# Performance work log

Measured on AMD Instinct MI355X. Metric: run time of the kernel, lower is better.

The kernel has to match this reference:

```python
import jax, jax.numpy as jnp
import numpy as np

B, N, D, H_DIM = 8, 100, 768, 768
TH = 24            # 384 / patch16
IMG = 384


def setup_inputs() -> dict:
    key = jax.random.key(0)
    k0, k1, k2, k3 = jax.random.split(key, 4)
    patch_tokens = jax.random.normal(k0, (B, TH * TH + 1, D), jnp.float32)
    raw = jax.random.uniform(k1, (B, N, 4), jnp.float32)
    x1 = jnp.minimum(raw[..., 0], raw[..., 2])
    x2 = jnp.maximum(raw[..., 0], raw[..., 2])
    y1 = jnp.minimum(raw[..., 1], raw[..., 3])
    y2 = jnp.maximum(raw[..., 1], raw[..., 3])
    boxes = jnp.stack([x1, y1, x2, y2], axis=-1)
    W1 = jax.random.normal(k2, (2 * D, H_DIM), jnp.float32) * 0.02
    b1 = jnp.zeros((H_DIM,), jnp.float32)
    W2 = jax.random.normal(k3, (H_DIM, 1), jnp.float32) * 0.02
    b2 = jnp.zeros((1,), jnp.float32)
    return {"patch_tokens": patch_tokens, "boxes": boxes, "W1": W1, "b1": b1,
            "W2": W2, "b2": b2, "img_h": IMG, "img_w": IMG}


def reference(patch_tokens, boxes, W1, b1, W2, b2, img_h, img_w):
    Bt, T, Dm = patch_tokens.shape
    th = int(T ** 0.5)                       # token_hw (24 for T=577)
    seq = patch_tokens[:, 1:, :] if T == th * th + 1 else patch_tokens
    feat_map = seq.reshape(Bt, th, th, Dm)   # [B, th, th, D]

    # --- box -> patch-grid coordinates (replicates int() truncation chain) ---
    def to_patch(v, size):
        pix = jnp.floor(v * size)            # int(x * W), x >= 0
        return jnp.floor(pix / size * th).astype(jnp.int32)

    px1 = jnp.clip(to_patch(boxes[..., 0], img_w), 0, th - 1)  # [B, N]
    py1 = jnp.clip(to_patch(boxes[..., 1], img_h), 0, th - 1)
    px2 = jnp.clip(to_patch(boxes[..., 2], img_w), 1, th)
    py2 = jnp.clip(to_patch(boxes[..., 3], img_h), 1, th)
    # empty-region fallback: single cell at (py1, px1)
    px2 = jnp.where(px2 > px1, px2, px1 + 1)
    py2 = jnp.where(py2 > py1, py2, py1 + 1)

    # --- vectorized ROI mean pooling via rectangle masks ---
    ar = jnp.arange(th)
    mx = (ar[None, None, :] >= px1[..., None]) & (ar[None, None, :] < px2[..., None])  # [B,N,th]
    my = (ar[None, None, :] >= py1[..., None]) & (ar[None, None, :] < py2[..., None])  # [B,N,th]
    mask = (my[..., :, None] & mx[..., None, :]).astype(feat_map.dtype)               # [B,N,th,th]
    count = mask.sum(axis=(-1, -2))                                                   # [B,N]
    pooled = jnp.einsum('bnhw,bhwd->bnd', mask, feat_map) / count[..., None]          # [B,N,D]

    # --- pairwise concat-MLP: cat([fi, fj]) @ W1 == fi @ W1[:D] + fj @ W1[D:] ---
    ha = pooled @ W1[:Dm]                     # [B,N,H]
    hb = pooled @ W1[Dm:]                     # [B,N,H]
    hid = jax.nn.relu(ha[:, :, None, :] + hb[:, None, :, :] + b1)  # [B,N,N,H]
    logits = (hid @ W2)[..., 0] + b2[0]       # [B,N,N]
    return jax.nn.sigmoid(logits)
```

## Files before the change

kernel.cpp:

```cpp
#include <hip/hip_runtime.h>
#include <hip/hip_bf16.h>
#include <math.h>

#define PB   8
#define PN   100
#define PD   768
#define PT   577
#define PTH  24
#define BN_TOT (PB * PN)
#define MPAD   832

typedef __attribute__((ext_vector_type(8))) short bf16x8;
typedef __attribute__((ext_vector_type(4))) float f32x4;

#define SATX_BLOCKS 144
#define CVT_BLOCKS  1152

__global__ __launch_bounds__(256) void prep_kernel(
    const float* __restrict__ patch,
    const float* __restrict__ W1,
    float* __restrict__ SAT,
    __hip_bfloat16* __restrict__ W1T)
{
    __shared__ float tile[32][33];
    const int t = threadIdx.x;

    if (blockIdx.x < SATX_BLOCKS) {
        const int gid = blockIdx.x * 256 + t;
        const int d4 = gid % 192;
        const int y  = (gid / 192) % PTH;
        const int b  = gid / (192 * PTH);

        const float4* src = (const float4*)(patch + ((size_t)(b * PT + 1 + y * PTH)) * PD) + d4;
        float4* dst = (float4*)(SAT + ((size_t)((b * 25) + (y + 1)) * 25) * PD) + d4;

        dst[0] = make_float4(0.f, 0.f, 0.f, 0.f);
        float4 acc = make_float4(0.f, 0.f, 0.f, 0.f);
#pragma unroll
        for (int X = 1; X <= PTH; ++X) {
            float4 v = src[(size_t)(X - 1) * 192];
            acc.x += v.x; acc.y += v.y; acc.z += v.z; acc.w += v.w;
            dst[(size_t)X * 192] = acc;
        }
    } else {
        const int bid = blockIdx.x - SATX_BLOCKS;
        const int half = bid / 576;
        const int rem  = bid % 576;
        const int k0 = (rem / 24) * 32;
        const int n0 = (rem % 24) * 32;
        const int c  = t & 31;
        const int r4 = t >> 5;

#pragma unroll
        for (int l = 0; l < 4; ++l) {
            int r = r4 + 8 * l;
            tile[r][c] = W1[(size_t)(half * PD + k0 + r) * PD + n0 + c];
        }
        __syncthreads();
#pragma unroll
        for (int l = 0; l < 4; ++l) {
            int r = r4 + 8 * l;
            W1T[(size_t)(half * PD + n0 + r) * PD + k0 + c] =
                __float2bfloat16(tile[c][r]);
        }
    }
}

__global__ __launch_bounds__(256) void sat_y_kernel(float* __restrict__ SAT)
{
    const int gid = blockIdx.x * 256 + threadIdx.x;
    const int d4 = gid % 192;
    const int X  = (gid / 192) % 25;
    const int b  = gid / (192 * 25);

    float4* col = (float4*)(SAT + ((size_t)(b * 25) * 25 + X) * PD) + d4;
    col[0] = make_float4(0.f, 0.f, 0.f, 0.f);
    float4 acc = make_float4(0.f, 0.f, 0.f, 0.f);
#pragma unroll
    for (int Y = 1; Y <= PTH; ++Y) {
        float4* p = col + (size_t)Y * 25 * 192;
        float4 v = *p;
        acc.x += v.x; acc.y += v.y; acc.z += v.z; acc.w += v.w;
        *p = acc;
    }
}

__global__ __launch_bounds__(192) void pool_sat_kernel(
    const float* __restrict__ SAT,
    const float* __restrict__ boxes,
    const int*   __restrict__ img_h,
    const int*   __restrict__ img_w,
    __hip_bfloat16* __restrict__ pooledh)
{
    const int m = blockIdx.x;
    const int t = threadIdx.x;
    short4* o = (short4*)(pooledh + (size_t)m * PD);

    if (m >= BN_TOT) {
        short4 z; z.x = 0; z.y = 0; z.z = 0; z.w = 0;
        o[t] = z;
        return;
    }

    const int b = m / PN;
    const float x1 = boxes[m * 4 + 0];
    const float y1 = boxes[m * 4 + 1];
    const float x2 = boxes[m * 4 + 2];
    const float y2 = boxes[m * 4 + 3];
    const float W  = (float)img_w[0];
    const float H  = (float)img_h[0];

    auto to_patch = [](float v, float size) -> int {
        float pix = floorf(v * size);
        float tt  = pix / size * (float)PTH;
        return (int)floorf(tt);
    };
    int px1 = min(max(to_patch(x1, W), 0), PTH - 1);
    int py1 = min(max(to_patch(y1, H), 0), PTH - 1);
    int px2 = min(max(to_patch(x2, W), 1), PTH);
    int py2 = min(max(to_patch(y2, H), 1), PTH);
    if (px2 <= px1) px2 = px1 + 1;
    if (py2 <= py1) py2 = py1 + 1;
    const float inv = 1.0f / (float)((px2 - px1) * (py2 - py1));

    const float* Sb = SAT + (size_t)b * 25 * 25 * PD;
    const float4 s22 = ((const float4*)(Sb + ((size_t)py2 * 25 + px2) * PD))[t];
    const float4 s12 = ((const float4*)(Sb + ((size_t)py1 * 25 + px2) * PD))[t];
    const float4 s21 = ((const float4*)(Sb + ((size_t)py2 * 25 + px1) * PD))[t];
    const float4 s11 = ((const float4*)(Sb + ((size_t)py1 * 25 + px1) * PD))[t];

    auto cvt = [](float f) -> short {
        __hip_bfloat16 h = __float2bfloat16(f);
        return *(short*)&h;
    };
    short4 r;
    r.x = cvt(((s22.x - s12.x) - (s21.x - s11.x)) * inv);
    r.y = cvt(((s22.y - s12.y) - (s21.y - s11.y)) * inv);
    r.z = cvt(((s22.z - s12.z) - (s21.z - s11.z)) * inv);
    r.w = cvt(((s22.w - s12.w) - (s21.w - s11.w)) * inv);
    o[t] = r;
}

__global__ __launch_bounds__(128) void gemm_mfma_kernel(
    const __hip_bfloat16* __restrict__ A,
    const __hip_bfloat16* __restrict__ Bt,
    const float* __restrict__ b1,
    float* __restrict__ C)
{
    const int bn = blockIdx.x;
    const int bm = blockIdx.y;
    const int wave = threadIdx.x >> 6;
    const int lane = threadIdx.x & 63;
    const int lm = lane & 15;
    const int g  = lane >> 4;

    const int m0 = bm * 32;
    const int n0 = bn * 64 + wave * 32;

    const __hip_bfloat16* pa0 = A  + (size_t)(m0 + lm) * PD + g * 8;
    const __hip_bfloat16* pa1 = pa0 + (size_t)16 * PD;
    const __hip_bfloat16* pb0 = Bt + (size_t)(n0 + lm) * PD + g * 8;
    const __hip_bfloat16* pb1 = pb0 + (size_t)16 * PD;

    f32x4 acc00 = {}, acc01 = {}, acc10 = {}, acc11 = {};

#pragma unroll 4
    for (int k0 = 0; k0 < PD; k0 += 32) {
        bf16x8 a0 = *(const bf16x8*)(pa0 + k0);
        bf16x8 a1 = *(const bf16x8*)(pa1 + k0);
        bf16x8 b0 = *(const bf16x8*)(pb0 + k0);
        bf16x8 b1v = *(const bf16x8*)(pb1 + k0);
        acc00 = __builtin_amdgcn_mfma_f32_16x16x32_bf16(a0, b0,  acc00, 0, 0, 0);
        acc01 = __builtin_amdgcn_mfma_f32_16x16x32_bf16(a0, b1v, acc01, 0, 0, 0);
        acc10 = __builtin_amdgcn_mfma_f32_16x16x32_bf16(a1, b0,  acc10, 0, 0, 0);
        acc11 = __builtin_amdgcn_mfma_f32_16x16x32_bf16(a1, b1v, acc11, 0, 0, 0);
    }

    const int rbase = g * 4;
#pragma unroll
    for (int r = 0; r < 4; ++r) {
        int row0 = m0 + rbase + r;
        int row1 = row0 + 16;
        int col0 = n0 + lm;
        int col1 = col0 + 16;
        float bb0 = (col0 < PD) ? b1[col0] : 0.0f;
        float bb1 = (col1 < PD) ? b1[col1] : 0.0f;
        C[(size_t)row0 * 1536 + col0] = acc00[r] + bb0;
        C[(size_t)row0 * 1536 + col1] = acc01[r] + bb1;
        C[(size_t)row1 * 1536 + col0] = acc10[r] + bb0;
        C[(size_t)row1 * 1536 + col1] = acc11[r] + bb1;
    }
}

__device__ __forceinline__ float rdot(const float4 A, const float4 C,
                                      const float4 W, float s) {
    s = fmaf(fmaxf(A.x + C.x, 0.f), W.x, s);
    s = fmaf(fmaxf(A.y + C.y, 0.f), W.y, s);
    s = fmaf(fmaxf(A.z + C.z, 0.f), W.z, s);
    s = fmaf(fmaxf(A.w + C.w, 0.f), W.w, s);
    return s;
}

__global__ __launch_bounds__(256) void pair_kernel(
    const float* __restrict__ hab,
    const float* __restrict__ W2,
    const float* __restrict__ b2,
    float* __restrict__ out)
{
    const int jt = blockIdx.x;
    const int i0 = blockIdx.y * 8;
    const int b  = blockIdx.z;
    const int nrows = min(8, PN - i0);
    const int t = threadIdx.x;
    const int wave = t >> 6;
    const int lane = t & 63;

    const float4* w2v = (const float4*)W2;
    const float4 w0 = w2v[lane], w1 = w2v[lane + 64], w2r = w2v[lane + 128];
    const float bb2 = b2[0];

    float4 a[8][3];
#pragma unroll
    for (int i = 0; i < 8; ++i) {
        int row = b * PN + (i < nrows ? i0 + i : i0);
        const float4* ha = (const float4*)(hab + (size_t)row * 1536);
        a[i][0] = ha[lane]; a[i][1] = ha[lane + 64]; a[i][2] = ha[lane + 128];
    }

    const float4* hbbase = (const float4*)(hab + (size_t)(b * PN) * 1536) + 192;
    const int jend = jt * 50 + 50;
    int j = jt * 50 + wave;

    float4 h0, h1, h2;
    {
        const float4* hb = hbbase + (size_t)j * 384;
        h0 = hb[lane]; h1 = hb[lane + 64]; h2 = hb[lane + 128];
    }

    for (; j < jend; j += 4) {
        const float4 c0 = h0, c1 = h1, c2 = h2;
        const int jn = j + 4;
        if (jn < jend) {
            const float4* hb = hbbase + (size_t)jn * 384;
            h0 = hb[lane]; h1 = hb[lane + 64]; h2 = hb[lane + 128];
        }
        float acc[8];
#pragma unroll
        for (int i = 0; i < 8; ++i)
            acc[i] = rdot(a[i][2], c2, w2r, rdot(a[i][1], c1, w1, rdot(a[i][0], c0, w0, 0.f)));
#pragma unroll
        for (int i = 0; i < 8; ++i)
#pragma unroll
            for (int m = 32; m; m >>= 1)
                acc[i] += __shfl_xor(acc[i], m, 64);
        if (lane == 0) {
#pragma unroll
            for (int i = 0; i < 8; ++i)
                if (i < nrows)
                    out[(size_t)(b * PN + i0 + i) * PN + j] =
                        1.0f / (1.0f + expf(-(acc[i] + bb2)));
        }
    }
}

extern "C" void kernel_launch(void* const* d_in, const int* in_sizes, int n_in,
                              void* d_out, int out_size, void* d_ws, size_t ws_size,
                              hipStream_t stream) {
    const float* patch = (const float*)d_in[0];
    const float* boxes = (const float*)d_in[1];
    const float* W1    = (const float*)d_in[2];
    const float* b1    = (const float*)d_in[3];
    const float* W2    = (const float*)d_in[4];
    const float* b2    = (const float*)d_in[5];
    const int*   img_h = (const int*)d_in[6];
    const int*   img_w = (const int*)d_in[7];
    float* out = (float*)d_out;

    char* wsb = (char*)d_ws;
    float*          SAT     = (float*)(wsb);
    __hip_bfloat16* pooledh = (__hip_bfloat16*)(wsb + 15360000);
    __hip_bfloat16* W1T     = (__hip_bfloat16*)(wsb + 15360000 + 1277952);
    float*          hab     = (float*)(wsb + 15360000 + 1277952 + 2359296);

    prep_kernel<<<SATX_BLOCKS + CVT_BLOCKS, 256, 0, stream>>>(patch, W1, SAT, W1T);
    sat_y_kernel<<<150, 256, 0, stream>>>(SAT);
    pool_sat_kernel<<<MPAD, 192, 0, stream>>>(SAT, boxes, img_h, img_w, pooledh);
    gemm_mfma_kernel<<<dim3(24, 26), 128, 0, stream>>>(pooledh, W1T, b1, hab);
    pair_kernel<<<dim3(2, 13, 8), 256, 0, stream>>>(hab, W2, b2, out);
}
```

Baseline: 137.5 us.

## Fuse all stages into one persistent kernel with grid-wide atomic barriers

Merges the prep, pooling, GEMM and pairwise kernels into a single persistent launch of 416 blocks, separated by software grid barriers built on atomic counters in the workspace. The counters are reset with a memset before each launch. The 2D summed-area table is replaced by row-wise prefix sums only, so each box is pooled by looping over its rows instead of using a four-corner lookup. The GEMM and pair stages are re-tiled so each fits the fixed block count. The change targets launch overhead and the separate vertical-scan pass, at the cost of barrier spin and the risk of deadlock if not all blocks are co-resident.

```diff
diff --git a/kernel.cpp b/kernel.cpp
--- a/kernel.cpp
+++ b/kernel.cpp
@@ -7,189 +7,38 @@
 #define PD   768
 #define PT   577
 #define PTH  24
-#define BN_TOT (PB * PN)
+#define BN_TOT 800
 #define MPAD   832
+
+#define NBLK 416
+#define NTHR 256
+#define TOTTHR (NBLK * NTHR)
 
 typedef __attribute__((ext_vector_type(8))) short bf16x8;
 typedef __attribute__((ext_vector_type(4))) float f32x4;
 
-#define SATX_BLOCKS 144
-#define CVT_BLOCKS  1152
-
-__global__ __launch_bounds__(256) void prep_kernel(
-    const float* __restrict__ patch,
-    const float* __restrict__ W1,
-    float* __restrict__ SAT,
-    __hip_bfloat16* __restrict__ W1T)
-{
-    __shared__ float tile[32][33];
-    const int t = threadIdx.x;
-
-    if (blockIdx.x < SATX_BLOCKS) {
-        const int gid = blockIdx.x * 256 + t;
-        const int d4 = gid % 192;
-        const int y  = (gid / 192) % PTH;
-        const int b  = gid / (192 * PTH);
-
-        const float4* src = (const float4*)(patch + ((size_t)(b * PT + 1 + y * PTH)) * PD) + d4;
-        float4* dst = (float4*)(SAT + ((size_t)((b * 25) + (y + 1)) * 25) * PD) + d4;
-
-        dst[0] = make_float4(0.f, 0.f, 0.f, 0.f);
-        float4 acc = make_float4(0.f, 0.f, 0.f, 0.f);
-#pragma unroll
-        for (int X = 1; X <= PTH; ++X) {
-            float4 v = src[(size_t)(X - 1) * 192];
-            acc.x += v.x; acc.y += v.y; acc.z += v.z; acc.w += v.w;
-            dst[(size_t)X * 192] = acc;
-        }
-    } else {
-        const int bid = blockIdx.x - SATX_BLOCKS;
-        const int half = bid / 576;
-        const int rem  = bid % 576;
-        const int k0 = (rem / 24) * 32;
-        const int n0 = (rem % 24) * 32;
-        const int c  = t & 31;
-        const int r4 = t >> 5;
-
-#pragma unroll
-        for (int l = 0; l < 4; ++l) {
-            int r = r4 + 8 * l;
-            tile[r][c] = W1[(size_t)(half * PD + k0 + r) * PD + n0 + c];
-        }
-        __syncthreads();
-#pragma unroll
-        for (int l = 0; l < 4; ++l) {
-            int r = r4 + 8 * l;
-            W1T[(size_t)(half * PD + n0 + r) * PD + k0 + c] =
-                __float2bfloat16(tile[c][r]);
-        }
-    }
-}
-
-__global__ __launch_bounds__(256) void sat_y_kernel(float* __restrict__ SAT)
-{
-    const int gid = blockIdx.x * 256 + threadIdx.x;
-    const int d4 = gid % 192;
-    const int X  = (gid / 192) % 25;
-    const int b  = gid / (192 * 25);
-
-    float4* col = (float4*)(SAT + ((size_t)(b * 25) * 25 + X) * PD) + d4;
-    col[0] = make_float4(0.f, 0.f, 0.f, 0.f);
-    float4 acc = make_float4(0.f, 0.f, 0.f, 0.f);
-#pragma unroll
-    for (int Y = 1; Y <= PTH; ++Y) {
-        float4* p = col + (size_t)Y * 25 * 192;
-        float4 v = *p;
-        acc.x += v.x; acc.y += v.y; acc.z += v.z; acc.w += v.w;
-        *p = acc;
-    }
-}
-
-__global__ __launch_bounds__(192) void pool_sat_kernel(
-    const float* __restrict__ SAT,
-    const float* __restrict__ boxes,
-    const int*   __restrict__ img_h,
-    const int*   __restrict__ img_w,
-    __hip_bfloat16* __restrict__ pooledh)
-{
-    const int m = blockIdx.x;
-    const int t = threadIdx.x;
-    short4* o = (short4*)(pooledh + (size_t)m * PD);
-
-    if (m >= BN_TOT) {
-        short4 z; z.x = 0; z.y = 0; z.z = 0; z.w = 0;
-        o[t] = z;
-        return;
-    }
-
-    const int b = m / PN;
-    const float x1 = boxes[m * 4 + 0];
-    const float y1 = boxes[m * 4 + 1];
-    const float x2 = boxes[m * 4 + 2];
-    const float y2 = boxes[m * 4 + 3];
-    const float W  = (float)img_w[0];
-    const float H  = (float)img_h[0];
-
-    auto to_patch = [](float v, float size) -> int {
-        float pix = floorf(v * size);
-        float tt  = pix / size * (float)PTH;
-        return (int)floorf(tt);
-    };
-    int px1 = min(max(to_patch(x1, W), 0), PTH - 1);
-    int py1 = min(max(to_patch(y1, H), 0), PTH - 1);
-    int px2 = min(max(to_patch(x2, W), 1), PTH);
-    int py2 = min(max(to_patch(y2, H), 1), PTH);
-    if (px2 <= px1) px2 = px1 + 1;
-    if (py2 <= py1) py2 = py1 + 1;
-    const float inv = 1.0f / (float)((px2 - px1) * (py2 - py1));
-
-    const float* Sb = SAT + (size_t)b * 25 * 25 * PD;
-    const float4 s22 = ((const float4*)(Sb + ((size_t)py2 * 25 + px2) * PD))[t];
-    const float4 s12 = ((const float4*)(Sb + ((size_t)py1 * 25 + px2) * PD))[t];
-    const float4 s21 = ((const float4*)(Sb + ((size_t)py2 * 25 + px1) * PD))[t];
-    const float4 s11 = ((const float4*)(Sb + ((size_t)py1 * 25 + px1) * PD))[t];
-
-    auto cvt = [](float f) -> short {
-        __hip_bfloat16 h = __float2bfloat16(f);
-        return *(short*)&h;
-    };
-    short4 r;
-    r.x = cvt(((s22.x - s12.x) - (s21.x - s11.x)) * inv);
-    r.y = cvt(((s22.y - s12.y) - (s21.y - s11.y)) * inv);
-    r.z = cvt(((s22.z - s12.z) - (s21.z - s11.z)) * inv);
-    r.w = cvt(((s22.w - s12.w) - (s21.w - s11.w)) * inv);
-    o[t] = r;
-}
-
-__global__ __launch_bounds__(128) void gemm_mfma_kernel(
-    const __hip_bfloat16* __restrict__ A,
-    const __hip_bfloat16* __restrict__ Bt,
-    const float* __restrict__ b1,
-    float* __restrict__ C)
-{
-    const int bn = blockIdx.x;
-    const int bm = blockIdx.y;
-    const int wave = threadIdx.x >> 6;
-    const int lane = threadIdx.x & 63;
-    const int lm = lane & 15;
-    const int g  = lane >> 4;
-
-    const int m0 = bm * 32;
-    const int n0 = bn * 64 + wave * 32;
-
-    const __hip_bfloat16* pa0 = A  + (size_t)(m0 + lm) * PD + g * 8;
-    const __hip_bfloat16* pa1 = pa0 + (size_t)16 * PD;
-    const __hip_bfloat16* pb0 = Bt + (size_t)(n0 + lm) * PD + g * 8;
-    const __hip_bfloat16* pb1 = pb0 + (size_t)16 * PD;
-
-    f32x4 acc00 = {}, acc01 = {}, acc10 = {}, acc11 = {};
-
-#pragma unroll 4
-    for (int k0 = 0; k0 < PD; k0 += 32) {
-        bf16x8 a0 = *(const bf16x8*)(pa0 + k0);
-        bf16x8 a1 = *(const bf16x8*)(pa1 + k0);
-        bf16x8 b0 = *(const bf16x8*)(pb0 + k0);
-        bf16x8 b1v = *(const bf16x8*)(pb1 + k0);
-        acc00 = __builtin_amdgcn_mfma_f32_16x16x32_bf16(a0, b0,  acc00, 0, 0, 0);
-        acc01 = __builtin_amdgcn_mfma_f32_16x16x32_bf16(a0, b1v, acc01, 0, 0, 0);
-        acc10 = __builtin_amdgcn_mfma_f32_16x16x32_bf16(a1, b0,  acc10, 0, 0, 0);
-        acc11 = __builtin_amdgcn_mfma_f32_16x16x32_bf16(a1, b1v, acc11, 0, 0, 0);
-    }
-
-    const int rbase = g * 4;
-#pragma unroll
-    for (int r = 0; r < 4; ++r) {
-        int row0 = m0 + rbase + r;
-        int row1 = row0 + 16;
-        int col0 = n0 + lm;
-        int col1 = col0 + 16;
-        float bb0 = (col0 < PD) ? b1[col0] : 0.0f;
-        float bb1 = (col1 < PD) ? b1[col1] : 0.0f;
-        C[(size_t)row0 * 1536 + col0] = acc00[r] + bb0;
-        C[(size_t)row0 * 1536 + col1] = acc01[r] + bb1;
-        C[(size_t)row1 * 1536 + col0] = acc10[r] + bb0;
-        C[(size_t)row1 * 1536 + col1] = acc11[r] + bb1;
-    }
+#define OFF_POOLED 14745600
+#define OFF_W1T    16023552
+#define OFF_HAB    18382848
+#define OFF_BAR    23494656
+
+__device__ __forceinline__ void gbar(unsigned* cnt, unsigned* flag) {
+    __syncthreads();
+    if (threadIdx.x == 0) {
+        __threadfence();
+        unsigned prev = __hip_atomic_fetch_add(cnt, 1u, __ATOMIC_ACQ_REL,
+                                               __HIP_MEMORY_SCOPE_AGENT);
+        if (prev == NBLK - 1) {
+            __hip_atomic_store(flag, 1u, __ATOMIC_RELEASE,
+                               __HIP_MEMORY_SCOPE_AGENT);
+        } else {
+            while (__hip_atomic_load(flag, __ATOMIC_ACQUIRE,
+                                     __HIP_MEMORY_SCOPE_AGENT) == 0u)
+                __builtin_amdgcn_s_sleep(2);
+        }
+        __threadfence();
+    }
+    __syncthreads();
 }
 
 __device__ __forceinline__ float rdot(const float4 A, const float4 C,
@@ -201,64 +50,218 @@
     return s;
 }
 
-__global__ __launch_bounds__(256) void pair_kernel(
-    const float* __restrict__ hab,
+__global__ __launch_bounds__(NTHR, 2) void fused_kernel(
+    const float* __restrict__ patch,
+    const float* __restrict__ boxes,
+    const float* __restrict__ W1,
+    const float* __restrict__ b1,
     const float* __restrict__ W2,
     const float* __restrict__ b2,
-    float* __restrict__ out)
+    const int*   __restrict__ img_h,
+    const int*   __restrict__ img_w,
+    float* __restrict__ out,
+    char* __restrict__ wsb)
 {
-    const int jt = blockIdx.x;
-    const int i0 = blockIdx.y * 8;
-    const int b  = blockIdx.z;
-    const int nrows = min(8, PN - i0);
-    const int t = threadIdx.x;
-    const int wave = t >> 6;
-    const int lane = t & 63;
-
-    const float4* w2v = (const float4*)W2;
-    const float4 w0 = w2v[lane], w1 = w2v[lane + 64], w2r = w2v[lane + 128];
-    const float bb2 = b2[0];
-
-    float4 a[8][3];
-#pragma unroll
-    for (int i = 0; i < 8; ++i) {
-        int row = b * PN + (i < nrows ? i0 + i : i0);
-        const float4* ha = (const float4*)(hab + (size_t)row * 1536);
-        a[i][0] = ha[lane]; a[i][1] = ha[lane + 64]; a[i][2] = ha[lane + 128];
-    }
-
-    const float4* hbbase = (const float4*)(hab + (size_t)(b * PN) * 1536) + 192;
-    const int jend = jt * 50 + 50;
-    int j = jt * 50 + wave;
-
-    float4 h0, h1, h2;
+    __shared__ float tile[32][33];
+
+    float*          Sx      = (float*)(wsb);
+    __hip_bfloat16* pooledh = (__hip_bfloat16*)(wsb + OFF_POOLED);
+    __hip_bfloat16* W1T     = (__hip_bfloat16*)(wsb + OFF_W1T);
+    float*          hab     = (float*)(wsb + OFF_HAB);
+    unsigned*       bar     = (unsigned*)(wsb + OFF_BAR);
+
+    const int bid = blockIdx.x;
+    const int t   = threadIdx.x;
+
+    if (bid < 144) {
+        const int gid = bid * 256 + t;
+        const int d4 = gid % 192;
+        const int y  = (gid / 192) % PTH;
+        const int b  = gid / (192 * PTH);
+
+        const float4* src = (const float4*)(patch +
+                            ((size_t)(b * PT + 1 + y * PTH)) * PD);
+        float4* dst = (float4*)(Sx + ((size_t)(b * PTH + y) * 25) * PD) + d4;
+
+        dst[0] = make_float4(0.f, 0.f, 0.f, 0.f);
+        float4 acc = make_float4(0.f, 0.f, 0.f, 0.f);
+#pragma unroll
+        for (int X = 1; X <= PTH; ++X) {
+            float4 v = src[(size_t)(X - 1) * 192 + d4];
+            acc.x += v.x; acc.y += v.y; acc.z += v.z; acc.w += v.w;
+            dst[(size_t)X * 192] = acc;
+        }
+    } else {
+        for (int tl = bid - 144; tl < 1152; tl += NBLK - 144) {
+            const int hf  = tl / 576;
+            const int rem = tl % 576;
+            const int k0 = (rem / 24) * 32;
+            const int n0 = (rem % 24) * 32;
+            const int c  = t & 31;
+            const int r4 = t >> 5;
+#pragma unroll
+            for (int l = 0; l < 4; ++l) {
+                int r = r4 + 8 * l;
+                tile[r][c] = W1[(size_t)(hf * PD + k0 + r) * PD + n0 + c];
+            }
+            __syncthreads();
+#pragma unroll
+            for (int l = 0; l < 4; ++l) {
+                int r = r4 + 8 * l;
+                W1T[(size_t)(hf * PD + n0 + r) * PD + k0 + c] =
+                    __float2bfloat16(tile[c][r]);
+            }
+            __syncthreads();
+        }
+    }
+    gbar(bar + 0, bar + 32);
+
     {
-        const float4* hb = hbbase + (size_t)j * 384;
-        h0 = hb[lane]; h1 = hb[lane + 64]; h2 = hb[lane + 128];
-    }
-
-    for (; j < jend; j += 4) {
-        const float4 c0 = h0, c1 = h1, c2 = h2;
-        const int jn = j + 4;
-        if (jn < jend) {
-            const float4* hb = hbbase + (size_t)jn * 384;
+        const float Wf = (float)img_w[0];
+        const float Hf = (float)img_h[0];
+        for (int u = bid * 256 + t; u < MPAD * 192; u += TOTTHR) {
+            const int m  = u / 192;
+            const int d4 = u % 192;
+            short4* o = (short4*)(pooledh + (size_t)m * PD) + d4;
+            if (m >= BN_TOT) {
+                short4 z; z.x = 0; z.y = 0; z.z = 0; z.w = 0;
+                *o = z;
+                continue;
+            }
+            const int b = m / PN;
+            auto to_patch = [](float v, float size) -> int {
+                float pix = floorf(v * size);
+                float tt  = pix / size * (float)PTH;
+                return (int)floorf(tt);
+            };
+            int px1 = min(max(to_patch(boxes[m * 4 + 0], Wf), 0), PTH - 1);
+            int py1 = min(max(to_patch(boxes[m * 4 + 1], Hf), 0), PTH - 1);
+            int px2 = min(max(to_patch(boxes[m * 4 + 2], Wf), 1), PTH);
+            int py2 = min(max(to_patch(boxes[m * 4 + 3], Hf), 1), PTH);
+            if (px2 <= px1) px2 = px1 + 1;
+            if (py2 <= py1) py2 = py1 + 1;
+            const float inv = 1.0f / (float)((px2 - px1) * (py2 - py1));
+
+            const float* Sb = Sx + (size_t)b * PTH * 25 * PD;
+            float4 s = make_float4(0.f, 0.f, 0.f, 0.f);
+            for (int y = py1; y < py2; ++y) {
+                const float4* r2 = (const float4*)(Sb + ((size_t)y * 25 + px2) * PD) + d4;
+                const float4* r1 = (const float4*)(Sb + ((size_t)y * 25 + px1) * PD) + d4;
+                float4 a2 = *r2, a1 = *r1;
+                s.x += a2.x - a1.x; s.y += a2.y - a1.y;
+                s.z += a2.z - a1.z; s.w += a2.w - a1.w;
+            }
+            auto cvt = [](float f) -> short {
+                __hip_bfloat16 h = __float2bfloat16(f);
+                return *(short*)&h;
+            };
+            short4 r;
+            r.x = cvt(s.x * inv); r.y = cvt(s.y * inv);
+            r.z = cvt(s.z * inv); r.w = cvt(s.w * inv);
+            *o = r;
+        }
+    }
+    gbar(bar + 64, bar + 96);
+
+    if (bid < 312) {
+        const int bm = bid / 24;
+        const int bn = bid % 24;
+        const int wave = t >> 6;
+        const int lane = t & 63;
+        const int lm = lane & 15;
+        const int g  = lane >> 4;
+        const int m0 = bm * 64 + (wave >> 1) * 32;
+        const int n0 = bn * 64 + (wave & 1) * 32;
+
+        const __hip_bfloat16* pa0 = pooledh + (size_t)(m0 + lm) * PD + g * 8;
+        const __hip_bfloat16* pa1 = pa0 + (size_t)16 * PD;
+        const __hip_bfloat16* pb0 = W1T + (size_t)(n0 + lm) * PD + g * 8;
+        const __hip_bfloat16* pb1 = pb0 + (size_t)16 * PD;
+
+        f32x4 acc00 = {}, acc01 = {}, acc10 = {}, acc11 = {};
+#pragma unroll 4
+        for (int k0 = 0; k0 < PD; k0 += 32) {
+            bf16x8 a0 = *(const bf16x8*)(pa0 + k0);
+            bf16x8 a1 = *(const bf16x8*)(pa1 + k0);
+            bf16x8 b0 = *(const bf16x8*)(pb0 + k0);
+            bf16x8 b1v = *(const bf16x8*)(pb1 + k0);
+            acc00 = __builtin_amdgcn_mfma_f32_16x16x32_bf16(a0, b0,  acc00, 0, 0, 0);
+            acc01 = __builtin_amdgcn_mfma_f32_16x16x32_bf16(a0, b1v, acc01, 0, 0, 0);
+            acc10 = __builtin_amdgcn_mfma_f32_16x16x32_bf16(a1, b0,  acc10, 0, 0, 0);
+            acc11 = __builtin_amdgcn_mfma_f32_16x16x32_bf16(a1, b1v, acc11, 0, 0, 0);
+        }
+        const int rbase = g * 4;
+#pragma unroll
+        for (int r = 0; r < 4; ++r) {
+            int row0 = m0 + rbase + r;
+            int row1 = row0 + 16;
+            int col0 = n0 + lm;
+            int col1 = col0 + 16;
+            float bb0 = (col0 < PD) ? b1[col0] : 0.0f;
+            float bb1 = (col1 < PD) ? b1[col1] : 0.0f;
+            hab[(size_t)row0 * 1536 + col0] = acc00[r] + bb0;
+            hab[(size_t)row0 * 1536 + col1] = acc01[r] + bb1;
+            hab[(size_t)row1 * 1536 + col0] = acc10[r] + bb0;
+            hab[(size_t)row1 * 1536 + col1] = acc11[r] + bb1;
+        }
+    }
+    gbar(bar + 128, bar + 160);
+
+    {
+        const int jt = bid & 3;
+        const int it = (bid >> 2) % 13;
+        const int b  = bid / 52;
+        const int i0 = it * 8;
+        const int nrows = min(8, PN - i0);
+        const int wave = t >> 6;
+        const int lane = t & 63;
+
+        const float4* w2v = (const float4*)W2;
+        const float4 w0 = w2v[lane], w1 = w2v[lane + 64], w2r = w2v[lane + 128];
+        const float bb2 = b2[0];
+
+        float4 a[8][3];
+#pragma unroll
+        for (int i = 0; i < 8; ++i) {
+            int row = b * PN + (i < nrows ? i0 + i : i0);
+            const float4* ha = (const float4*)(hab + (size_t)row * 1536);
+            a[i][0] = ha[lane]; a[i][1] = ha[lane + 64]; a[i][2] = ha[lane + 128];
+        }
+
+        const float4* hbbase = (const float4*)(hab + (size_t)(b * PN) * 1536) + 192;
+        const int jend = jt * 25 + 25;
+        int j = jt * 25 + wave;
+
+        float4 h0, h1, h2;
+        {
+            const float4* hb = hbbase + (size_t)j * 384;
             h0 = hb[lane]; h1 = hb[lane + 64]; h2 = hb[lane + 128];
         }
-        float acc[8];
-#pragma unroll
-        for (int i = 0; i < 8; ++i)
-            acc[i] = rdot(a[i][2], c2, w2r, rdot(a[i][1], c1, w1, rdot(a[i][0], c0, w0, 0.f)));
-#pragma unroll
-        for (int i = 0; i < 8; ++i)
-#pragma unroll
-            for (int m = 32; m; m >>= 1)
-                acc[i] += __shfl_xor(acc[i], m, 64);
-        if (lane == 0) {
+        for (; j < jend; j += 4) {
+            const float4 c0 = h0, c1 = h1, c2 = h2;
+            const int jn = j + 4;
+            if (jn < jend) {
+                const float4* hb = hbbase + (size_t)jn * 384;
+                h0 = hb[lane]; h1 = hb[lane + 64]; h2 = hb[lane + 128];
+            }
+            float acc[8];
 #pragma unroll
             for (int i = 0; i < 8; ++i)
-                if (i < nrows)
-                    out[(size_t)(b * PN + i0 + i) * PN + j] =
-                        1.0f / (1.0f + expf(-(acc[i] + bb2)));
+                acc[i] = rdot(a[i][2], c2, w2r,
+                         rdot(a[i][1], c1, w1,
+                         rdot(a[i][0], c0, w0, 0.f)));
+#pragma unroll
+            for (int i = 0; i < 8; ++i)
+#pragma unroll
+                for (int m = 32; m; m >>= 1)
+                    acc[i] += __shfl_xor(acc[i], m, 64);
+            if (lane == 0) {
+#pragma unroll
+                for (int i = 0; i < 8; ++i)
+                    if (i < nrows)
+                        out[(size_t)(b * PN + i0 + i) * PN + j] =
+                            1.0f / (1.0f + expf(-(acc[i] + bb2)));
+            }
         }
     }
 }
@@ -275,16 +278,9 @@
     const int*   img_h = (const int*)d_in[6];
     const int*   img_w = (const int*)d_in[7];
     float* out = (float*)d_out;
-
     char* wsb = (char*)d_ws;
-    float*          SAT     = (float*)(wsb);
-    __hip_bfloat16* pooledh = (__hip_bfloat16*)(wsb + 15360000);
-    __hip_bfloat16* W1T     = (__hip_bfloat16*)(wsb + 15360000 + 1277952);
-    float*          hab     = (float*)(wsb + 15360000 + 1277952 + 2359296);
-
-    prep_kernel<<<SATX_BLOCKS + CVT_BLOCKS, 256, 0, stream>>>(patch, W1, SAT, W1T);
-    sat_y_kernel<<<150, 256, 0, stream>>>(SAT);
-    pool_sat_kernel<<<MPAD, 192, 0, stream>>>(SAT, boxes, img_h, img_w, pooledh);
-    gemm_mfma_kernel<<<dim3(24, 26), 128, 0, stream>>>(pooledh, W1T, b1, hab);
-    pair_kernel<<<dim3(2, 13, 8), 256, 0, stream>>>(hab, W2, b2, out);
-}
+
+    hipMemsetAsync(wsb + OFF_BAR, 0, 1024, stream);
+    fused_kernel<<<NBLK, NTHR, 0, stream>>>(patch, boxes, W1, b1, W2, b2,
+                                            img_h, img_w, out, wsb);
+}
```

Measured after the change: 358.0 us. +160.4%, slower.

## Replace SAT pooling with direct box summation fused into W1 conversion kernel

Applied to the files above, without the earlier changes.

Drops the two-pass summed-area-table build (SAT x and y kernels plus the separate pool kernel) and sums each box's patch tokens directly inside one kernel. That kernel also carries the W1 transpose/bf16 conversion as a grid-stride loop, cutting three launches down to one and removing the 15 MB SAT workspace traffic. The pair kernel's j-range is split into 4 chunks instead of 2, doubling its grid for more parallelism. The trade-off is that direct summation costs work proportional to box area: large boxes can read up to 576 tokens each, which may load-imbalance blocks.

```diff
diff --git a/kernel.cpp b/kernel.cpp
--- a/kernel.cpp
+++ b/kernel.cpp
@@ -7,138 +7,88 @@
 #define PD   768
 #define PT   577
 #define PTH  24
-#define BN_TOT (PB * PN)
+#define BN_TOT 800
 #define MPAD   832
 
 typedef __attribute__((ext_vector_type(8))) short bf16x8;
 typedef __attribute__((ext_vector_type(4))) float f32x4;
 
-#define SATX_BLOCKS 144
-#define CVT_BLOCKS  1152
-
-__global__ __launch_bounds__(256) void prep_kernel(
+__global__ __launch_bounds__(256) void pool_prep_kernel(
     const float* __restrict__ patch,
+    const float* __restrict__ boxes,
     const float* __restrict__ W1,
-    float* __restrict__ SAT,
+    const int*   __restrict__ img_h,
+    const int*   __restrict__ img_w,
+    __hip_bfloat16* __restrict__ pooledh,
     __hip_bfloat16* __restrict__ W1T)
 {
     __shared__ float tile[32][33];
+    const int m = blockIdx.x;
     const int t = threadIdx.x;
 
-    if (blockIdx.x < SATX_BLOCKS) {
-        const int gid = blockIdx.x * 256 + t;
-        const int d4 = gid % 192;
-        const int y  = (gid / 192) % PTH;
-        const int b  = gid / (192 * PTH);
-
-        const float4* src = (const float4*)(patch + ((size_t)(b * PT + 1 + y * PTH)) * PD) + d4;
-        float4* dst = (float4*)(SAT + ((size_t)((b * 25) + (y + 1)) * 25) * PD) + d4;
-
-        dst[0] = make_float4(0.f, 0.f, 0.f, 0.f);
-        float4 acc = make_float4(0.f, 0.f, 0.f, 0.f);
-#pragma unroll
-        for (int X = 1; X <= PTH; ++X) {
-            float4 v = src[(size_t)(X - 1) * 192];
-            acc.x += v.x; acc.y += v.y; acc.z += v.z; acc.w += v.w;
-            dst[(size_t)X * 192] = acc;
-        }
-    } else {
-        const int bid = blockIdx.x - SATX_BLOCKS;
-        const int half = bid / 576;
-        const int rem  = bid % 576;
+    if (t < 192) {
+        short4* o = (short4*)(pooledh + (size_t)m * PD) + t;
+        if (m >= BN_TOT) {
+            short4 z; z.x = 0; z.y = 0; z.z = 0; z.w = 0;
+            *o = z;
+        } else {
+            const int b = m / PN;
+            const float Wf = (float)img_w[0];
+            const float Hf = (float)img_h[0];
+            auto to_patch = [](float v, float size) -> int {
+                float pix = floorf(v * size);
+                float tt  = pix / size * (float)PTH;
+                return (int)floorf(tt);
+            };
+            int px1 = min(max(to_patch(boxes[m * 4 + 0], Wf), 0), PTH - 1);
+            int py1 = min(max(to_patch(boxes[m * 4 + 1], Hf), 0), PTH - 1);
+            int px2 = min(max(to_patch(boxes[m * 4 + 2], Wf), 1), PTH);
+            int py2 = min(max(to_patch(boxes[m * 4 + 3], Hf), 1), PTH);
+            if (px2 <= px1) px2 = px1 + 1;
+            if (py2 <= py1) py2 = py1 + 1;
+            const float inv = 1.0f / (float)((px2 - px1) * (py2 - py1));
+
+            const float* pb_ = patch + (size_t)(b * PT + 1) * PD;
+            float4 s = make_float4(0.f, 0.f, 0.f, 0.f);
+            for (int y = py1; y < py2; ++y) {
+                const float* rowp = pb_ + (size_t)(y * PTH) * PD;
+                for (int x = px1; x < px2; ++x) {
+                    float4 v = ((const float4*)(rowp + (size_t)x * PD))[t];
+                    s.x += v.x; s.y += v.y; s.z += v.z; s.w += v.w;
+                }
+            }
+            auto cvt = [](float f) -> short {
+                __hip_bfloat16 h = __float2bfloat16(f);
+                return *(short*)&h;
+            };
+            short4 r;
+            r.x = cvt(s.x * inv); r.y = cvt(s.y * inv);
+            r.z = cvt(s.z * inv); r.w = cvt(s.w * inv);
+            *o = r;
+        }
+    }
+
+    for (int tl = m; tl < 1152; tl += MPAD) {
+        const int hf  = tl / 576;
+        const int rem = tl % 576;
         const int k0 = (rem / 24) * 32;
         const int n0 = (rem % 24) * 32;
         const int c  = t & 31;
         const int r4 = t >> 5;
-
+        __syncthreads();
 #pragma unroll
         for (int l = 0; l < 4; ++l) {
             int r = r4 + 8 * l;
-            tile[r][c] = W1[(size_t)(half * PD + k0 + r) * PD + n0 + c];
+            tile[r][c] = W1[(size_t)(hf * PD + k0 + r) * PD + n0 + c];
         }
         __syncthreads();
 #pragma unroll
         for (int l = 0; l < 4; ++l) {
             int r = r4 + 8 * l;
-            W1T[(size_t)(half * PD + n0 + r) * PD + k0 + c] =
+            W1T[(size_t)(hf * PD + n0 + r) * PD + k0 + c] =
                 __float2bfloat16(tile[c][r]);
         }
     }
-}
-
-__global__ __launch_bounds__(256) void sat_y_kernel(float* __restrict__ SAT)
-{
-    const int gid = blockIdx.x * 256 + threadIdx.x;
-    const int d4 = gid % 192;
-    const int X  = (gid / 192) % 25;
-    const int b  = gid / (192 * 25);
-
-    float4* col = (float4*)(SAT + ((size_t)(b * 25) * 25 + X) * PD) + d4;
-    col[0] = make_float4(0.f, 0.f, 0.f, 0.f);
-    float4 acc = make_float4(0.f, 0.f, 0.f, 0.f);
-#pragma unroll
-    for (int Y = 1; Y <= PTH; ++Y) {
-        float4* p = col + (size_t)Y * 25 * 192;
-        float4 v = *p;
-        acc.x += v.x; acc.y += v.y; acc.z += v.z; acc.w += v.w;
-        *p = acc;
-    }
-}
-
-__global__ __launch_bounds__(192) void pool_sat_kernel(
-    const float* __restrict__ SAT,
-    const float* __restrict__ boxes,
-    const int*   __restrict__ img_h,
-    const int*   __restrict__ img_w,
-    __hip_bfloat16* __restrict__ pooledh)
-{
-    const int m = blockIdx.x;
-    const int t = threadIdx.x;
-    short4* o = (short4*)(pooledh + (size_t)m * PD);
-
-    if (m >= BN_TOT) {
-        short4 z; z.x = 0; z.y = 0; z.z = 0; z.w = 0;
-        o[t] = z;
-        return;
-    }
-
-    const int b = m / PN;
-    const float x1 = boxes[m * 4 + 0];
-    const float y1 = boxes[m * 4 + 1];
-    const float x2 = boxes[m * 4 + 2];
-    const float y2 = boxes[m * 4 + 3];
-    const float W  = (float)img_w[0];
-    const float H  = (float)img_h[0];
-
-    auto to_patch = [](float v, float size) -> int {
-        float pix = floorf(v * size);
-        float tt  = pix / size * (float)PTH;
-        return (int)floorf(tt);
-    };
-    int px1 = min(max(to_patch(x1, W), 0), PTH - 1);
-    int py1 = min(max(to_patch(y1, H), 0), PTH - 1);
-    int px2 = min(max(to_patch(x2, W), 1), PTH);
-    int py2 = min(max(to_patch(y2, H), 1), PTH);
-    if (px2 <= px1) px2 = px1 + 1;
-    if (py2 <= py1) py2 = py1 + 1;
-    const float inv = 1.0f / (float)((px2 - px1) * (py2 - py1));
-
-    const float* Sb = SAT + (size_t)b * 25 * 25 * PD;
-    const float4 s22 = ((const float4*)(Sb + ((size_t)py2 * 25 + px2) * PD))[t];
-    const float4 s12 = ((const float4*)(Sb + ((size_t)py1 * 25 + px2) * PD))[t];
-    const float4 s21 = ((const float4*)(Sb + ((size_t)py2 * 25 + px1) * PD))[t];
-    const float4 s11 = ((const float4*)(Sb + ((size_t)py1 * 25 + px1) * PD))[t];
-
-    auto cvt = [](float f) -> short {
-        __hip_bfloat16 h = __float2bfloat16(f);
-        return *(short*)&h;
-    };
-    short4 r;
-    r.x = cvt(((s22.x - s12.x) - (s21.x - s11.x)) * inv);
-    r.y = cvt(((s22.y - s12.y) - (s21.y - s11.y)) * inv);
-    r.z = cvt(((s22.z - s12.z) - (s21.z - s11.z)) * inv);
-    r.w = cvt(((s22.w - s12.w) - (s21.w - s11.w)) * inv);
-    o[t] = r;
 }
 
 __global__ __launch_bounds__(128) void gemm_mfma_kernel(
@@ -228,15 +178,14 @@
     }
 
     const float4* hbbase = (const float4*)(hab + (size_t)(b * PN) * 1536) + 192;
-    const int jend = jt * 50 + 50;
-    int j = jt * 50 + wave;
+    const int jend = jt * 25 + 25;
+    int j = jt * 25 + wave;
 
     float4 h0, h1, h2;
     {
         const float4* hb = hbbase + (size_t)j * 384;
         h0 = hb[lane]; h1 = hb[lane + 64]; h2 = hb[lane + 128];
     }
-
     for (; j < jend; j += 4) {
         const float4 c0 = h0, c1 = h1, c2 = h2;
         const int jn = j + 4;
@@ -247,7 +196,9 @@
         float acc[8];
 #pragma unroll
         for (int i = 0; i < 8; ++i)
-            acc[i] = rdot(a[i][2], c2, w2r, rdot(a[i][1], c1, w1, rdot(a[i][0], c0, w0, 0.f)));
+            acc[i] = rdot(a[i][2], c2, w2r,
+                     rdot(a[i][1], c1, w1,
+                     rdot(a[i][0], c0, w0, 0.f)));
 #pragma unroll
         for (int i = 0; i < 8; ++i)
 #pragma unroll
@@ -277,14 +228,12 @@
     float* out = (float*)d_out;
 
     char* wsb = (char*)d_ws;
-    float*          SAT     = (float*)(wsb);
-    __hip_bfloat16* pooledh = (__hip_bfloat16*)(wsb + 15360000);
-    __hip_bfloat16* W1T     = (__hip_bfloat16*)(wsb + 15360000 + 1277952);
-    float*          hab     = (float*)(wsb + 15360000 + 1277952 + 2359296);
-
-    prep_kernel<<<SATX_BLOCKS + CVT_BLOCKS, 256, 0, stream>>>(patch, W1, SAT, W1T);
-    sat_y_kernel<<<150, 256, 0, stream>>>(SAT);
-    pool_sat_kernel<<<MPAD, 192, 0, stream>>>(SAT, boxes, img_h, img_w, pooledh);
+    __hip_bfloat16* pooledh = (__hip_bfloat16*)(wsb);
+    __hip_bfloat16* W1T     = (__hip_bfloat16*)(wsb + 1277952);
+    float*          hab     = (float*)(wsb + 3637248);
+
+    pool_prep_kernel<<<MPAD, 256, 0, stream>>>(patch, boxes, W1, img_h, img_w,
+                                               pooledh, W1T);
     gemm_mfma_kernel<<<dim3(24, 26), 128, 0, stream>>>(pooledh, W1T, b1, hab);
-    pair_kernel<<<dim3(2, 13, 8), 256, 0, stream>>>(hab, W2, b2, out);
-}
+    pair_kernel<<<dim3(4, 13, 8), 256, 0, stream>>>(hab, W2, b2, out);
+}
```

Result: slower. 206.7 us (+50.3%).
